# Optimization experiments

Hardware: AMD Instinct MI355X
Metric: run time of the kernel (lower is better)

Reference implementation:

```python
import jax, jax.numpy as jnp
import numpy as np

# Config derived from layers=[1024,1024,1024,1024,1024]
B = 16384      # batch
H1 = 1024      # layers[1], width of first odd layer (Ux target slice)
SE = 2048      # sum of even-layer dims (0 + 1024 + 1024)
SO = 2048      # sum of odd-layer dims (1024 + 1024)
LAYER = 1024
N_STEPS = 10


def rho(x):
    return jax.nn.sigmoid(4.0 * (x - 0.5))


def rhod(x):
    r = rho(x)
    return 4.0 * r * (1.0 - r)


def _block_mask():
    # Staircase blocks per layer_slices(): (0:1024,0:1024), (0:1024,1024:2048), (1024:2048,1024:2048)
    m = np.zeros((SE, SO), dtype=np.float32)
    m[0:LAYER, 0:LAYER] = 1.0
    m[0:LAYER, LAYER:2 * LAYER] = 1.0
    m[LAYER:2 * LAYER, LAYER:2 * LAYER] = 1.0
    return jnp.asarray(m)


def setup_inputs() -> dict:
    key = jax.random.key(0)
    k1, k2, k3, k4, k5 = jax.random.split(key, 5)
    Ux = jax.random.normal(k1, (B, H1), dtype=jnp.float32)
    s = jax.random.normal(k2, (B, SE + SO), dtype=jnp.float32)
    # Xavier uniform per 1024x1024 block: bound = sqrt(6 / (1024 + 1024))
    bound = (6.0 / (2 * LAYER)) ** 0.5
    W = jax.random.uniform(k3, (SE, SO), minval=-bound, maxval=bound, dtype=jnp.float32) * _block_mask()
    b_even = 0.01 * jax.random.normal(k4, (1, SE), dtype=jnp.float32)
    b_odd = 0.01 * jax.random.normal(k5, (1, SO), dtype=jnp.float32)
    return {"Ux": Ux, "s": s, "W": W, "b_even": b_even, "b_odd": b_odd}


def reference(Ux, s, W, b_even, b_odd):
    s_even, s_odd = s[:, :SE], s[:, SE:]
    # C_odd = rho(s_even) @ W + b_odd ; first odd layer also receives Ux
    C_odd = rho(s_even) @ W + b_odd
    C_odd = C_odd.at[:, :H1].add(Ux)
    for _ in range(N_STEPS):
        s_odd = 0.5 * s_odd + 0.5 * rhod(s_odd) * C_odd
    C_even = rho(s_odd) @ W.T + b_even
    for _ in range(N_STEPS):
        s_even = 0.5 * s_even + 0.5 * rhod(s_even) * C_even
    return jnp.concatenate([s_even, s_odd], axis=-1)
```

## Files before the change

kernel.cpp:

```cpp
#include <hip/hip_runtime.h>
#include <hip/hip_bf16.h>

#define BATCH 16384
#define SEW   2048
#define H1W   1024
#define NSTEP 10

typedef unsigned short u16;
typedef __attribute__((ext_vector_type(8))) __bf16 bf16x8;
typedef __attribute__((ext_vector_type(4))) float   f32x4;

__device__ __forceinline__ void split2(float x, u16& h, u16& l) {
    unsigned u = __float_as_uint(x);
    h = (u16)(u >> 16);
    float hf = __uint_as_float(u & 0xFFFF0000u);
    float r  = x - hf;
    l = (u16)(__float_as_uint(r) >> 16);
}

__device__ __forceinline__ float rho_f(float x) {
    return 1.0f / (1.0f + __expf(2.0f - 4.0f * x));
}

__device__ __forceinline__ void gl2lds16(const u16* g, u16* l) {
    __builtin_amdgcn_global_load_lds(
        (const __attribute__((address_space(1))) void*)g,
        (__attribute__((address_space(3))) void*)l, 16, 0, 0);
}

__global__ void prep_w(const float* __restrict__ W,
                       u16* __restrict__ Whi, u16* __restrict__ Wlo,
                       u16* __restrict__ WThi, u16* __restrict__ WTlo) {
    __shared__ float tile[32][33];
    const int tx = threadIdx.x, ty = threadIdx.y;
    const int x = blockIdx.x * 32 + tx;
#pragma unroll
    for (int k = 0; k < 4; ++k) {
        int y = blockIdx.y * 32 + ty + k * 8;
        float v = W[y * SEW + x];
        tile[ty + k * 8][tx] = v;
        u16 h, l; split2(v, h, l);
        Whi[y * SEW + x] = h; Wlo[y * SEW + x] = l;
    }
    __syncthreads();
#pragma unroll
    for (int k = 0; k < 4; ++k) {
        int r = blockIdx.x * 32 + ty + k * 8;
        int c = blockIdx.y * 32 + tx;
        float v = tile[tx][ty + k * 8];
        u16 h, l; split2(v, h, l);
        WThi[r * SEW + c] = h; WTlo[r * SEW + c] = l;
    }
}

__global__ void prep_rho(const float* __restrict__ s,
                         u16* __restrict__ Rhi, u16* __restrict__ Rlo) {
    int i = blockIdx.x * blockDim.x + threadIdx.x;
    int e = i << 2;
    int row = e >> 11;
    int col = e & 2047;
    const float4 v = *(const float4*)(s + ((size_t)row << 12) + col);
    float xs[4] = {v.x, v.y, v.z, v.w};
    u16 h[4], l[4];
#pragma unroll
    for (int k = 0; k < 4; ++k) {
        float r = rho_f(xs[k]);
        split2(r, h[k], l[k]);
    }
    *(ushort4*)(Rhi + e) = make_ushort4(h[0], h[1], h[2], h[3]);
    *(ushort4*)(Rlo + e) = make_ushort4(l[0], l[1], l[2], l[3]);
}

template <int PHASE>
__global__ __launch_bounds__(512, 2)
void gemm_fused(const u16* __restrict__ Ahi, const u16* __restrict__ Alo,
                const u16* __restrict__ Bhi, const u16* __restrict__ Blo,
                const float* __restrict__ bias,
                const float* __restrict__ Ux,
                const float* __restrict__ s_in,
                float* __restrict__ out,
                u16* __restrict__ R2hi, u16* __restrict__ R2lo) {
    __shared__ u16 ldsA[2][256 * 64];
    __shared__ u16 ldsB[2][256 * 64];

    const int tid = threadIdx.x;

    const int wg = blockIdx.x;
    const int L  = (wg & 7) * 64 + (wg >> 3);
    const int m0 = (L >> 3) * 256;
    const int n0 = (L & 7) * 256;

    int kt0, nkt;
    if (PHASE == 1) { kt0 = 0;                    nkt = (n0 < 1024) ? 16 : 32; }
    else            { kt0 = (n0 < 1024) ? 0 : 16; nkt = (n0 < 1024) ? 32 : 16; }
    const int nvt = 3 * nkt;

    const int srow  = tid >> 3;
    const int sswz  = (tid >> 4) & 7;
    const int scol  = ((tid & 7) ^ sswz) * 8;
    const int aoff0 = (m0 + srow) * SEW + scol;
    const int boff0 = (n0 + srow) * SEW + scol;

    const int lane = tid & 63;
    const int w  = tid >> 6;
    const int wr = w >> 2, wc = w & 3;
    const int lr = lane & 15, q = lane >> 4;
    const int swz = (lr >> 1) & 7;
    const int oh0 = ((q)     ^ swz) * 16;
    const int oh1 = ((4 + q) ^ swz) * 16;
    const int baseA = (wr * 128 + lr) * 128;
    const int baseB = (wc * 64  + lr) * 128;

    f32x4 acc[8][4];
    const f32x4 zero = {0.f, 0.f, 0.f, 0.f};
#pragma unroll
    for (int i = 0; i < 8; ++i)
#pragma unroll
        for (int j = 0; j < 4; ++j) acc[i][j] = zero;

#define STAGE(As, Bs, kk, buf) do {                                          \
        u16* dA_ = &ldsA[buf][tid * 8];                                      \
        u16* dB_ = &ldsB[buf][tid * 8];                                      \
        const u16* sa_ = (As) + aoff0 + (kk);                                \
        const u16* sb_ = (Bs) + boff0 + (kk);                                \
        _Pragma("unroll")                                                    \
        for (int i_ = 0; i_ < 4; ++i_) {                                     \
            gl2lds16(sa_ + i_ * (64 * SEW), dA_ + i_ * 4096);                \
            gl2lds16(sb_ + i_ * (64 * SEW), dB_ + i_ * 4096);                \
        }                                                                    \
    } while (0)

    int skk = kt0 * 64;
    int st  = 1;
    STAGE(Ahi, Bhi, skk, 0);

    for (int vt = 0; vt < nvt; ++vt) {
        const int cur = vt & 1;
        if (vt + 1 < nvt) {
            const u16* As = (st < 2)  ? Ahi : Alo;
            const u16* Bs = (st == 1) ? Blo : Bhi;
            STAGE(As, Bs, skk, cur ^ 1);
            if (++st == 3) { st = 0; skk += 64; }
            asm volatile("s_waitcnt vmcnt(8)" ::: "memory");
        } else {
            asm volatile("s_waitcnt vmcnt(0)" ::: "memory");
        }
        __builtin_amdgcn_s_barrier();

        const char* la = (const char*)ldsA[cur];
        const char* lb = (const char*)ldsB[cur];
        bf16x8 av[4][2], bv[4][2];
#pragma unroll
        for (int i = 0; i < 4; ++i) {
            av[i][0] = *(const bf16x8*)(la + baseA + i * 2048 + oh0);
            av[i][1] = *(const bf16x8*)(la + baseA + i * 2048 + oh1);
        }
#pragma unroll
        for (int j = 0; j < 4; ++j) {
            bv[j][0] = *(const bf16x8*)(lb + baseB + j * 2048 + oh0);
            bv[j][1] = *(const bf16x8*)(lb + baseB + j * 2048 + oh1);
        }
        __builtin_amdgcn_s_setprio(1);
#pragma unroll
        for (int i = 0; i < 4; ++i)
#pragma unroll
            for (int j = 0; j < 2; ++j) {
                acc[i][j] = __builtin_amdgcn_mfma_f32_16x16x32_bf16(av[i][0], bv[j][0], acc[i][j], 0, 0, 0);
                acc[i][j] = __builtin_amdgcn_mfma_f32_16x16x32_bf16(av[i][1], bv[j][1], acc[i][j], 0, 0, 0);
            }
        __builtin_amdgcn_s_setprio(0);
        __builtin_amdgcn_s_setprio(1);
#pragma unroll
        for (int i = 0; i < 4; ++i)
#pragma unroll
            for (int j = 2; j < 4; ++j) {
                acc[i][j] = __builtin_amdgcn_mfma_f32_16x16x32_bf16(av[i][0], bv[j][0], acc[i][j], 0, 0, 0);
                acc[i][j] = __builtin_amdgcn_mfma_f32_16x16x32_bf16(av[i][1], bv[j][1], acc[i][j], 0, 0, 0);
            }
        __builtin_amdgcn_s_setprio(0);
#pragma unroll
        for (int i = 0; i < 4; ++i) {
            av[i][0] = *(const bf16x8*)(la + baseA + (i + 4) * 2048 + oh0);
            av[i][1] = *(const bf16x8*)(la + baseA + (i + 4) * 2048 + oh1);
        }
        __builtin_amdgcn_s_setprio(1);
#pragma unroll
        for (int i = 0; i < 4; ++i)
#pragma unroll
            for (int j = 0; j < 2; ++j) {
                acc[4 + i][j] = __builtin_amdgcn_mfma_f32_16x16x32_bf16(av[i][0], bv[j][0], acc[4 + i][j], 0, 0, 0);
                acc[4 + i][j] = __builtin_amdgcn_mfma_f32_16x16x32_bf16(av[i][1], bv[j][1], acc[4 + i][j], 0, 0, 0);
            }
        __builtin_amdgcn_s_setprio(0);
        __builtin_amdgcn_s_setprio(1);
#pragma unroll
        for (int i = 0; i < 4; ++i)
#pragma unroll
            for (int j = 2; j < 4; ++j) {
                acc[4 + i][j] = __builtin_amdgcn_mfma_f32_16x16x32_bf16(av[i][0], bv[j][0], acc[4 + i][j], 0, 0, 0);
                acc[4 + i][j] = __builtin_amdgcn_mfma_f32_16x16x32_bf16(av[i][1], bv[j][1], acc[4 + i][j], 0, 0, 0);
            }
        __builtin_amdgcn_s_setprio(0);

        __builtin_amdgcn_s_barrier();
    }
#undef STAGE

#pragma unroll
    for (int i = 0; i < 8; ++i) {
#pragma unroll
        for (int j = 0; j < 4; ++j) {
            const int col = n0 + wc * 64 + j * 16 + lr;
            const float bvv = bias[col];
            float c[4], sv[4];
#pragma unroll
            for (int jj = 0; jj < 4; ++jj) {
                const int row = m0 + wr * 128 + i * 16 + q * 4 + jj;
                c[jj] = acc[i][j][jj] + bvv;
                if (PHASE == 1) {
                    if (n0 < 1024) c[jj] += Ux[(size_t)row * H1W + col];
                }
                sv[jj] = s_in[(size_t)row * 4096 + col];
            }
#pragma unroll 1
            for (int t = 0; t < NSTEP; ++t) {
#pragma unroll
                for (int jj = 0; jj < 4; ++jj) {
                    float r  = rho_f(sv[jj]);
                    float rd = 4.0f * r * (1.0f - r);
                    sv[jj] = 0.5f * sv[jj] + 0.5f * rd * c[jj];
                }
            }
#pragma unroll
            for (int jj = 0; jj < 4; ++jj) {
                const int row = m0 + wr * 128 + i * 16 + q * 4 + jj;
                out[(size_t)row * 4096 + col] = sv[jj];
                if (PHASE == 1) {
                    float r = rho_f(sv[jj]);
                    u16 h, l; split2(r, h, l);
                    R2hi[(size_t)row * SEW + col] = h;
                    R2lo[(size_t)row * SEW + col] = l;
                }
            }
        }
    }
}

extern "C" void kernel_launch(void* const* d_in, const int* in_sizes, int n_in,
                              void* d_out, int out_size, void* d_ws, size_t ws_size,
                              hipStream_t stream) {
    (void)in_sizes; (void)n_in; (void)out_size; (void)ws_size;
    const float* Ux     = (const float*)d_in[0];
    const float* s      = (const float*)d_in[1];
    const float* W      = (const float*)d_in[2];
    const float* b_even = (const float*)d_in[3];
    const float* b_odd  = (const float*)d_in[4];
    float* out = (float*)d_out;

    char* ws = (char*)d_ws;
    const size_t MB = 1024ull * 1024ull;
    u16* R1hi = (u16*)(ws);
    u16* R1lo = (u16*)(ws + 64 * MB);
    u16* R2hi = (u16*)(ws + 128 * MB);
    u16* R2lo = (u16*)(ws + 192 * MB);
    u16* Whi  = (u16*)(ws + 256 * MB);
    u16* Wlo  = (u16*)(ws + 264 * MB);
    u16* WThi = (u16*)(ws + 272 * MB);
    u16* WTlo = (u16*)(ws + 280 * MB);

    prep_w<<<dim3(64, 64), dim3(32, 8), 0, stream>>>(W, Whi, Wlo, WThi, WTlo);
    prep_rho<<<(BATCH * SEW / 4) / 256, 256, 0, stream>>>(s, R1hi, R1lo);

    gemm_fused<1><<<dim3(512), 512, 0, stream>>>(
        R1hi, R1lo, WThi, WTlo, b_odd, Ux,
        s + SEW, out + SEW, R2hi, R2lo);

    gemm_fused<2><<<dim3(512), 512, 0, stream>>>(
        R2hi, R2lo, Whi, Wlo, b_even, nullptr,
        s, out, nullptr, nullptr);
}
```

Baseline: 1.606 ms.

## Shrink GEMM tiles to 128x128x32 with 256-thread blocks and more workgroups

Reduces the fused GEMM output tile from 256x256 with K-step 64 to 128x128 with K-step 32, using 4 waves per block instead of 8 and launching 2048 blocks instead of 512. LDS per block shrinks, accumulators drop to 4x4 fragments, and occupancy is targeted at 3 blocks per CU. The aim is better load balance across CUs and more latency hiding. The cost is lower arithmetic intensity per tile, more global/L2 traffic for the A and B operands, and more barriers per unit of work.

```diff
diff --git a/kernel.cpp b/kernel.cpp
--- a/kernel.cpp
+++ b/kernel.cpp
@@ -72,7 +72,7 @@
 }
 
 template <int PHASE>
-__global__ __launch_bounds__(512, 2)
+__global__ __launch_bounds__(256, 3)
 void gemm_fused(const u16* __restrict__ Ahi, const u16* __restrict__ Alo,
                 const u16* __restrict__ Bhi, const u16* __restrict__ Blo,
                 const float* __restrict__ bias,
@@ -80,41 +80,43 @@
                 const float* __restrict__ s_in,
                 float* __restrict__ out,
                 u16* __restrict__ R2hi, u16* __restrict__ R2lo) {
-    __shared__ u16 ldsA[2][256 * 64];
-    __shared__ u16 ldsB[2][256 * 64];
+    __shared__ u16 ldsA[2][128 * 32];
+    __shared__ u16 ldsB[2][128 * 32];
 
     const int tid = threadIdx.x;
 
     const int wg = blockIdx.x;
-    const int L  = (wg & 7) * 64 + (wg >> 3);
-    const int m0 = (L >> 3) * 256;
-    const int n0 = (L & 7) * 256;
+    const int L  = (wg & 7) * 256 + (wg >> 3);
+    const int m0 = (L >> 4) * 128;
+    const int n0 = (L & 15) * 128;
 
     int kt0, nkt;
-    if (PHASE == 1) { kt0 = 0;                    nkt = (n0 < 1024) ? 16 : 32; }
-    else            { kt0 = (n0 < 1024) ? 0 : 16; nkt = (n0 < 1024) ? 32 : 16; }
+    if (PHASE == 1) { kt0 = 0;                    nkt = (n0 < 1024) ? 32 : 64; }
+    else            { kt0 = (n0 < 1024) ? 0 : 32; nkt = (n0 < 1024) ? 64 : 32; }
     const int nvt = 3 * nkt;
 
-    const int srow  = tid >> 3;
-    const int sswz  = (tid >> 4) & 7;
-    const int scol  = ((tid & 7) ^ sswz) * 8;
+    const int srow = tid >> 2;
+    const int sswz = (tid >> 3) & 3;
+    const int scol = ((tid & 3) ^ sswz) * 8;
     const int aoff0 = (m0 + srow) * SEW + scol;
     const int boff0 = (n0 + srow) * SEW + scol;
 
     const int lane = tid & 63;
     const int w  = tid >> 6;
-    const int wr = w >> 2, wc = w & 3;
+    const int wr = w >> 1, wc = w & 1;
     const int lr = lane & 15, q = lane >> 4;
-    const int swz = (lr >> 1) & 7;
-    const int oh0 = ((q)     ^ swz) * 16;
-    const int oh1 = ((4 + q) ^ swz) * 16;
-    const int baseA = (wr * 128 + lr) * 128;
-    const int baseB = (wc * 64  + lr) * 128;
-
-    f32x4 acc[8][4];
+    const int oh = ((q ^ ((lr >> 1) & 3))) << 4;
+    int offA[4], offB[4];
+#pragma unroll
+    for (int i = 0; i < 4; ++i) {
+        offA[i] = (wr * 64 + i * 16 + lr) * 64 + oh;
+        offB[i] = (wc * 64 + i * 16 + lr) * 64 + oh;
+    }
+
+    f32x4 acc[4][4];
     const f32x4 zero = {0.f, 0.f, 0.f, 0.f};
 #pragma unroll
-    for (int i = 0; i < 8; ++i)
+    for (int i = 0; i < 4; ++i)
 #pragma unroll
         for (int j = 0; j < 4; ++j) acc[i][j] = zero;
 
@@ -123,14 +125,13 @@
         u16* dB_ = &ldsB[buf][tid * 8];                                      \
         const u16* sa_ = (As) + aoff0 + (kk);                                \
         const u16* sb_ = (Bs) + boff0 + (kk);                                \
-        _Pragma("unroll")                                                    \
-        for (int i_ = 0; i_ < 4; ++i_) {                                     \
-            gl2lds16(sa_ + i_ * (64 * SEW), dA_ + i_ * 4096);                \
-            gl2lds16(sb_ + i_ * (64 * SEW), dB_ + i_ * 4096);                \
-        }                                                                    \
+        gl2lds16(sa_, dA_);                                                  \
+        gl2lds16(sa_ + 64 * SEW, dA_ + 2048);                                \
+        gl2lds16(sb_, dB_);                                                  \
+        gl2lds16(sb_ + 64 * SEW, dB_ + 2048);                                \
     } while (0)
 
-    int skk = kt0 * 64;
+    int skk = kt0 * 32;
     int st  = 1;
     STAGE(Ahi, Bhi, skk, 0);
 
@@ -140,8 +141,8 @@
             const u16* As = (st < 2)  ? Ahi : Alo;
             const u16* Bs = (st == 1) ? Blo : Bhi;
             STAGE(As, Bs, skk, cur ^ 1);
-            if (++st == 3) { st = 0; skk += 64; }
-            asm volatile("s_waitcnt vmcnt(8)" ::: "memory");
+            if (++st == 3) { st = 0; skk += 32; }
+            asm volatile("s_waitcnt vmcnt(4)" ::: "memory");
         } else {
             asm volatile("s_waitcnt vmcnt(0)" ::: "memory");
         }
@@ -149,65 +150,26 @@
 
         const char* la = (const char*)ldsA[cur];
         const char* lb = (const char*)ldsB[cur];
-        bf16x8 av[4][2], bv[4][2];
-#pragma unroll
-        for (int i = 0; i < 4; ++i) {
-            av[i][0] = *(const bf16x8*)(la + baseA + i * 2048 + oh0);
-            av[i][1] = *(const bf16x8*)(la + baseA + i * 2048 + oh1);
-        }
-#pragma unroll
-        for (int j = 0; j < 4; ++j) {
-            bv[j][0] = *(const bf16x8*)(lb + baseB + j * 2048 + oh0);
-            bv[j][1] = *(const bf16x8*)(lb + baseB + j * 2048 + oh1);
-        }
+        bf16x8 av[4], bv[4];
+#pragma unroll
+        for (int i = 0; i < 4; ++i) av[i] = *(const bf16x8*)(la + offA[i]);
+#pragma unroll
+        for (int j = 0; j < 4; ++j) bv[j] = *(const bf16x8*)(lb + offB[j]);
+
         __builtin_amdgcn_s_setprio(1);
 #pragma unroll
         for (int i = 0; i < 4; ++i)
 #pragma unroll
-            for (int j = 0; j < 2; ++j) {
-                acc[i][j] = __builtin_amdgcn_mfma_f32_16x16x32_bf16(av[i][0], bv[j][0], acc[i][j], 0, 0, 0);
-                acc[i][j] = __builtin_amdgcn_mfma_f32_16x16x32_bf16(av[i][1], bv[j][1], acc[i][j], 0, 0, 0);
-            }
+            for (int j = 0; j < 4; ++j)
+                acc[i][j] = __builtin_amdgcn_mfma_f32_16x16x32_bf16(av[i], bv[j], acc[i][j], 0, 0, 0);
         __builtin_amdgcn_s_setprio(0);
-        __builtin_amdgcn_s_setprio(1);
-#pragma unroll
-        for (int i = 0; i < 4; ++i)
-#pragma unroll
-            for (int j = 2; j < 4; ++j) {
-                acc[i][j] = __builtin_amdgcn_mfma_f32_16x16x32_bf16(av[i][0], bv[j][0], acc[i][j], 0, 0, 0);
-                acc[i][j] = __builtin_amdgcn_mfma_f32_16x16x32_bf16(av[i][1], bv[j][1], acc[i][j], 0, 0, 0);
-            }
-        __builtin_amdgcn_s_setprio(0);
-#pragma unroll
-        for (int i = 0; i < 4; ++i) {
-            av[i][0] = *(const bf16x8*)(la + baseA + (i + 4) * 2048 + oh0);
-            av[i][1] = *(const bf16x8*)(la + baseA + (i + 4) * 2048 + oh1);
-        }
-        __builtin_amdgcn_s_setprio(1);
-#pragma unroll
-        for (int i = 0; i < 4; ++i)
-#pragma unroll
-            for (int j = 0; j < 2; ++j) {
-                acc[4 + i][j] = __builtin_amdgcn_mfma_f32_16x16x32_bf16(av[i][0], bv[j][0], acc[4 + i][j], 0, 0, 0);
-                acc[4 + i][j] = __builtin_amdgcn_mfma_f32_16x16x32_bf16(av[i][1], bv[j][1], acc[4 + i][j], 0, 0, 0);
-            }
-        __builtin_amdgcn_s_setprio(0);
-        __builtin_amdgcn_s_setprio(1);
-#pragma unroll
-        for (int i = 0; i < 4; ++i)
-#pragma unroll
-            for (int j = 2; j < 4; ++j) {
-                acc[4 + i][j] = __builtin_amdgcn_mfma_f32_16x16x32_bf16(av[i][0], bv[j][0], acc[4 + i][j], 0, 0, 0);
-                acc[4 + i][j] = __builtin_amdgcn_mfma_f32_16x16x32_bf16(av[i][1], bv[j][1], acc[4 + i][j], 0, 0, 0);
-            }
-        __builtin_amdgcn_s_setprio(0);
 
         __builtin_amdgcn_s_barrier();
     }
 #undef STAGE
 
 #pragma unroll
-    for (int i = 0; i < 8; ++i) {
+    for (int i = 0; i < 4; ++i) {
 #pragma unroll
         for (int j = 0; j < 4; ++j) {
             const int col = n0 + wc * 64 + j * 16 + lr;
@@ -215,7 +177,7 @@
             float c[4], sv[4];
 #pragma unroll
             for (int jj = 0; jj < 4; ++jj) {
-                const int row = m0 + wr * 128 + i * 16 + q * 4 + jj;
+                const int row = m0 + wr * 64 + i * 16 + q * 4 + jj;
                 c[jj] = acc[i][j][jj] + bvv;
                 if (PHASE == 1) {
                     if (n0 < 1024) c[jj] += Ux[(size_t)row * H1W + col];
@@ -233,7 +195,7 @@
             }
 #pragma unroll
             for (int jj = 0; jj < 4; ++jj) {
-                const int row = m0 + wr * 128 + i * 16 + q * 4 + jj;
+                const int row = m0 + wr * 64 + i * 16 + q * 4 + jj;
                 out[(size_t)row * 4096 + col] = sv[jj];
                 if (PHASE == 1) {
                     float r = rho_f(sv[jj]);
@@ -271,11 +233,11 @@
     prep_w<<<dim3(64, 64), dim3(32, 8), 0, stream>>>(W, Whi, Wlo, WThi, WTlo);
     prep_rho<<<(BATCH * SEW / 4) / 256, 256, 0, stream>>>(s, R1hi, R1lo);
 
-    gemm_fused<1><<<dim3(512), 512, 0, stream>>>(
+    gemm_fused<1><<<dim3(2048), 256, 0, stream>>>(
         R1hi, R1lo, WThi, WTlo, b_odd, Ux,
         s + SEW, out + SEW, R2hi, R2lo);
 
-    gemm_fused<2><<<dim3(512), 512, 0, stream>>>(
+    gemm_fused<2><<<dim3(2048), 256, 0, stream>>>(
         R2hi, R2lo, Whi, Wlo, b_even, nullptr,
         s, out, nullptr, nullptr);
 }
```

Result: faster. 1.556 ms (-3.1%).
